# Kernel optimization log

Hardware: AMD Instinct MI355X
Metric: run time of the kernel (lower is better)

The kernel has to match this reference:

```python
import jax, jax.numpy as jnp
import numpy as np

B, S, D, E, H = 65536, 4, 128, 128, 4
HD = E // H
EPS = 1e-5


def setup_inputs() -> dict:
    key = jax.random.key(0)
    ks = jax.random.split(key, 20)
    sc = 0.05
    return {
        'h0': jax.random.normal(ks[0], (B, D), jnp.float32),
        'h1': jax.random.normal(ks[1], (B, D), jnp.float32),
        'h2': jax.random.normal(ks[2], (B, D), jnp.float32),
        'h3': jax.random.normal(ks[3], (B, D), jnp.float32),
        'proj_w': jax.random.normal(ks[4], (S, D, E), jnp.float32) * sc,
        'proj_b': jax.random.normal(ks[5], (S, E), jnp.float32) * sc,
        'ctx_w': jax.random.normal(ks[6], (E,), jnp.float32) * sc,
        'ctx_b': jax.random.normal(ks[7], (), jnp.float32) * sc,
        'in_proj_w': jax.random.normal(ks[8], (E, 3 * E), jnp.float32) * sc,
        'in_proj_b': jax.random.normal(ks[9], (3 * E,), jnp.float32) * sc,
        'out_w': jax.random.normal(ks[10], (E, E), jnp.float32) * sc,
        'out_b': jax.random.normal(ks[11], (E,), jnp.float32) * sc,
        'gate_w': jax.random.normal(ks[12], (2 * E, E), jnp.float32) * sc,
        'gate_b': jax.random.normal(ks[13], (E,), jnp.float32) * sc,
        'pool_w': jax.random.normal(ks[14], (E,), jnp.float32) * sc,
        'pool_b': jax.random.normal(ks[15], (), jnp.float32) * sc,
        'ln_g': jnp.ones((E,), jnp.float32),
        'ln_b': jnp.zeros((E,), jnp.float32),
    }


def reference(h0, h1, h2, h3, proj_w, proj_b, ctx_w, ctx_b, in_proj_w, in_proj_b,
              out_w, out_b, gate_w, gate_b, pool_w, pool_b, ln_g, ln_b):
    hs = jnp.stack([h0, h1, h2, h3], axis=1)                      # [B,S,D]
    x = jnp.einsum('bsd,sde->bse', hs, proj_w) + proj_b           # [B,S,E]
    # context attention over sources
    cw = jax.nn.softmax(x @ ctx_w + ctx_b, axis=1)                # [B,S]
    context = jnp.einsum('bse,bs->be', x, cw)                     # [B,E]
    # single-query MHA: query=context, keys/vals=x
    wq, wk, wv = jnp.split(in_proj_w, 3, axis=1)
    bq, bk, bv = jnp.split(in_proj_b, 3)
    q = (context @ wq + bq).reshape(B, H, HD)
    k = (x @ wk + bk).reshape(B, S, H, HD)
    v = (x @ wv + bv).reshape(B, S, H, HD)
    scores = jnp.einsum('bhd,bshd->bhs', q, k) / jnp.sqrt(jnp.float32(HD))
    attn = jax.nn.softmax(scores, axis=-1)                        # [B,H,S]
    o = jnp.einsum('bhs,bshd->bhd', attn, v).reshape(B, E)
    attn_out = o @ out_w + out_b                                  # [B,E]
    attn_weights = jnp.mean(attn, axis=1)[:, None, :]             # [B,1,S] (avg heads)
    ao = jnp.broadcast_to(attn_out[:, None, :], (B, S, E))
    gate_in = jnp.concatenate([x, ao], axis=-1)                   # [B,S,2E]
    g = jax.nn.sigmoid(gate_in @ gate_w + gate_b)                 # [B,S,E]
    fused = g * ao + (1.0 - g) * x
    mu = fused.mean(axis=-1, keepdims=True)
    var = fused.var(axis=-1, keepdims=True)
    fused = (fused - mu) * jax.lax.rsqrt(var + EPS) * ln_g + ln_b
    pw = jax.nn.softmax(fused @ pool_w + pool_b, axis=1)          # [B,S]
    pooled = jnp.einsum('bse,bs->be', fused, pw)                  # [B,E]
    return pooled, attn_weights, g
```

## Files before the change

kernel.cpp:

```cpp
#include <hip/hip_runtime.h>
#include <hip/hip_bf16.h>

typedef unsigned short u16;
typedef unsigned int   u32;
typedef short  short8 __attribute__((ext_vector_type(8)));
typedef float  f32x4  __attribute__((ext_vector_type(4)));

#define NB    65536
#define XP    132
#define OFF1  ((size_t)NB * 128)
#define OFF2  (OFF1 + (size_t)NB * 4)

__device__ __forceinline__ u16 f2bf(float f) {
  __hip_bfloat16 b = __float2bfloat16(f);
  u16 u; __builtin_memcpy(&u, &b, 2); return u;
}
__device__ __forceinline__ float bf2f(u32 bits16) {
  union { u32 u; float f; } v; v.u = bits16 << 16; return v.f;
}
__device__ __forceinline__ float red16(float v) {
  v += __shfl_xor(v, 1); v += __shfl_xor(v, 2);
  v += __shfl_xor(v, 4); v += __shfl_xor(v, 8);
  return v;
}
__device__ __forceinline__ void lds_fence() {
  asm volatile("s_waitcnt lgkmcnt(0)" ::: "memory");
}

__global__ void pack_w(const float* __restrict__ proj_w,
                       const float* __restrict__ in_proj_w,
                       const float* __restrict__ out_w,
                       const float* __restrict__ gate_w,
                       u16* __restrict__ wp) {
  int t = blockIdx.x * 256 + threadIdx.x;
  if (t >= 10 * 16384) return;
  int w = t >> 14, i = t & 16383;
  int nt = i >> 11, kt = (i >> 9) & 3, ln = (i >> 3) & 63, j = i & 7;
  int k = kt * 32 + ((ln >> 4) << 3) + j;
  int n = (nt << 4) + (ln & 15);
  float v;
  if (w < 4)       v = proj_w[((size_t)w << 14) + (k << 7) + n];
  else if (w < 7)  v = in_proj_w[k * 384 + ((w - 4) << 7) + n];
  else if (w == 7) v = out_w[(k << 7) + n];
  else             v = gate_w[(((w - 8) << 7) + k) * 128 + n];
  wp[t] = f2bf(v);
}

__device__ __forceinline__ short8 bfrag(const u16* __restrict__ wp, int w, int nt, int kt, int lane) {
  return *(const short8*)(wp + ((size_t)w << 14) + (size_t)((((nt << 2) + kt) << 6) + lane) * 8);
}

struct AF { short8 a[4]; };
__device__ __forceinline__ AF loadA(const u16 (*Ab)[XP], int row, int lgrp) {
  AF r;
  #pragma unroll
  for (int kt = 0; kt < 4; ++kt)
    r.a[kt] = *(const short8*)&Ab[row][kt * 32 + (lgrp << 3)];
  return r;
}
__device__ __forceinline__ f32x4 mmK128(const AF& A, const u16* __restrict__ wp, int w,
                                        int ntg, int lane, float bias) {
  f32x4 acc = {bias, bias, bias, bias};
  #pragma unroll
  for (int kt = 0; kt < 4; ++kt)
    acc = __builtin_amdgcn_mfma_f32_16x16x32_bf16(A.a[kt], bfrag(wp, w, ntg, kt, lane), acc, 0, 0, 0);
  return acc;
}

__global__ __launch_bounds__(64, 2) void fused_k(
    const float* __restrict__ h0, const float* __restrict__ h1,
    const float* __restrict__ h2, const float* __restrict__ h3,
    const u16* __restrict__ wp,
    const float* __restrict__ proj_b, const float* __restrict__ ctx_w,
    const float* __restrict__ in_proj_b, const float* __restrict__ out_b,
    const float* __restrict__ gate_b, const float* __restrict__ pool_w,
    const float* __restrict__ ln_g, const float* __restrict__ ln_b,
    float* __restrict__ out) {
  __shared__ __align__(16) u16 xls[4][16][XP];
  __shared__ __align__(16) u16 scr[16][XP];

  const int lane  = threadIdx.x;
  const int lrow  = lane & 15;
  const int lgrp  = lane >> 4;
  const int crow0 = lgrp << 2;
  const size_t r0w = (size_t)blockIdx.x * 16;

  const float* hp[4] = {h0, h1, h2, h3};

  float ctxl[4][4];
  #pragma unroll
  for (int s = 0; s < 4; ++s) {
    const float* __restrict__ hb = hp[s] + ((r0w + lrow) << 7) + (lgrp << 3);
    AF Ah;
    #pragma unroll
    for (int kt = 0; kt < 4; ++kt) {
      float4 va = *(const float4*)(hb + kt * 32);
      float4 vb = *(const float4*)(hb + kt * 32 + 4);
      short8 v;
      v[0] = (short)f2bf(va.x); v[1] = (short)f2bf(va.y);
      v[2] = (short)f2bf(va.z); v[3] = (short)f2bf(va.w);
      v[4] = (short)f2bf(vb.x); v[5] = (short)f2bf(vb.y);
      v[6] = (short)f2bf(vb.z); v[7] = (short)f2bf(vb.w);
      Ah.a[kt] = v;
    }
    float lp[4] = {0.f, 0.f, 0.f, 0.f};
    #pragma unroll
    for (int nt = 0; nt < 8; ++nt) {
      int n = (nt << 4) + lrow;
      f32x4 acc = mmK128(Ah, wp, s, nt, lane, proj_b[(s << 7) + n]);
      float cwn = ctx_w[n];
      #pragma unroll
      for (int j = 0; j < 4; ++j) {
        lp[j] += acc[j] * cwn;
        xls[s][crow0 + j][n] = f2bf(acc[j]);
      }
    }
    #pragma unroll
    for (int j = 0; j < 4; ++j) ctxl[s][j] = red16(lp[j]);
  }

  float cw[4][4];
  #pragma unroll
  for (int j = 0; j < 4; ++j) {
    float l0 = ctxl[0][j], l1 = ctxl[1][j], l2 = ctxl[2][j], l3 = ctxl[3][j];
    float mx = fmaxf(fmaxf(l0, l1), fmaxf(l2, l3));
    float e0 = __expf(l0 - mx), e1 = __expf(l1 - mx), e2 = __expf(l2 - mx), e3 = __expf(l3 - mx);
    float inv = 1.f / (e0 + e1 + e2 + e3);
    cw[0][j] = e0 * inv; cw[1][j] = e1 * inv; cw[2][j] = e2 * inv; cw[3][j] = e3 * inv;
  }
  #pragma unroll
  for (int nt = 0; nt < 8; ++nt) {
    int n = (nt << 4) + lrow;
    #pragma unroll
    for (int j = 0; j < 4; ++j) {
      float v = cw[0][j] * bf2f((u32)xls[0][crow0 + j][n])
              + cw[1][j] * bf2f((u32)xls[1][crow0 + j][n])
              + cw[2][j] * bf2f((u32)xls[2][crow0 + j][n])
              + cw[3][j] * bf2f((u32)xls[3][crow0 + j][n]);
      scr[crow0 + j][n] = f2bf(v);
    }
  }
  lds_fence();
  AF Ac = loadA(scr, lrow, lgrp);

  float qf[8][4];
  #pragma unroll
  for (int nt = 0; nt < 8; ++nt) {
    int n = (nt << 4) + lrow;
    f32x4 acc = mmK128(Ac, wp, 4, nt, lane, in_proj_b[n]);
    #pragma unroll
    for (int j = 0; j < 4; ++j) qf[nt][j] = acc[j];
  }

  lds_fence();
  AF Axs[4];
  #pragma unroll
  for (int s = 0; s < 4; ++s) Axs[s] = loadA(xls[s], lrow, lgrp);
  float sc[4][4][4] = {};
  #pragma unroll
  for (int nt = 0; nt < 8; ++nt) {
    int n = (nt << 4) + lrow;
    const int h = nt >> 1;
    float bk = in_proj_b[128 + n];
    f32x4 ak[4];
    #pragma unroll
    for (int s = 0; s < 4; ++s) ak[s] = (f32x4){bk, bk, bk, bk};
    #pragma unroll
    for (int kt = 0; kt < 4; ++kt) {
      short8 bf = bfrag(wp, 5, nt, kt, lane);
      #pragma unroll
      for (int s = 0; s < 4; ++s)
        ak[s] = __builtin_amdgcn_mfma_f32_16x16x32_bf16(Axs[s].a[kt], bf, ak[s], 0, 0, 0);
    }
    #pragma unroll
    for (int s = 0; s < 4; ++s)
      #pragma unroll
      for (int j = 0; j < 4; ++j)
        sc[s][j][h] += ak[s][j] * qf[nt][j];
  }
  #pragma unroll
  for (int s = 0; s < 4; ++s)
    #pragma unroll
    for (int j = 0; j < 4; ++j)
      #pragma unroll
      for (int h = 0; h < 4; ++h)
        sc[s][j][h] = red16(sc[s][j][h]);

  float aw[4][4][4];
  #pragma unroll
  for (int j = 0; j < 4; ++j)
    #pragma unroll
    for (int h = 0; h < 4; ++h) {
      const float scale = 0.17677669529663687f;
      float l0 = sc[0][j][h] * scale, l1 = sc[1][j][h] * scale;
      float l2 = sc[2][j][h] * scale, l3 = sc[3][j][h] * scale;
      float mx = fmaxf(fmaxf(l0, l1), fmaxf(l2, l3));
      float e0 = __expf(l0 - mx), e1 = __expf(l1 - mx), e2 = __expf(l2 - mx), e3 = __expf(l3 - mx);
      float inv = 1.f / (e0 + e1 + e2 + e3);
      aw[0][j][h] = e0 * inv; aw[1][j][h] = e1 * inv;
      aw[2][j][h] = e2 * inv; aw[3][j][h] = e3 * inv;
    }
  {
    float* awp = (float*)scr;
    if (lrow == 0) {
      #pragma unroll
      for (int s = 0; s < 4; ++s)
        #pragma unroll
        for (int j = 0; j < 4; ++j)
          awp[((crow0 + j) << 2) + s] =
            0.25f * (aw[s][j][0] + aw[s][j][1] + aw[s][j][2] + aw[s][j][3]);
    }
    lds_fence();
    out[OFF1 + (r0w << 2) + lane] = awp[lane];
  }

  {
    float oa[8][4] = {};
    #pragma unroll
    for (int nt = 0; nt < 8; ++nt) {
      int n = (nt << 4) + lrow;
      const int h = nt >> 1;
      float bv = in_proj_b[256 + n];
      f32x4 av[4];
      #pragma unroll
      for (int s = 0; s < 4; ++s) av[s] = (f32x4){bv, bv, bv, bv};
      #pragma unroll
      for (int kt = 0; kt < 4; ++kt) {
        short8 bf = bfrag(wp, 6, nt, kt, lane);
        #pragma unroll
        for (int s = 0; s < 4; ++s)
          av[s] = __builtin_amdgcn_mfma_f32_16x16x32_bf16(Axs[s].a[kt], bf, av[s], 0, 0, 0);
      }
      #pragma unroll
      for (int s = 0; s < 4; ++s)
        #pragma unroll
        for (int j = 0; j < 4; ++j)
          oa[nt][j] += aw[s][j][h] * av[s][j];
    }
    #pragma unroll
    for (int nt = 0; nt < 8; ++nt) {
      int n = (nt << 4) + lrow;
      #pragma unroll
      for (int j = 0; j < 4; ++j) scr[crow0 + j][n] = f2bf(oa[nt][j]);
    }
  }
  lds_fence();
  AF Ao = loadA(scr, lrow, lgrp);

  float aoreg[8][4];
  #pragma unroll
  for (int nt = 0; nt < 8; ++nt) {
    int n = (nt << 4) + lrow;
    f32x4 acc = mmK128(Ao, wp, 7, nt, lane, out_b[n]);
    #pragma unroll
    for (int j = 0; j < 4; ++j) {
      scr[crow0 + j][n] = f2bf(acc[j]);
      aoreg[nt][j] = acc[j];
    }
  }
  lds_fence();
  AF Aa = loadA(scr, lrow, lgrp);

  f32x4 aacc[8];
  #pragma unroll
  for (int nt = 0; nt < 8; ++nt) {
    int n = (nt << 4) + lrow;
    float gb = gate_b[n];
    f32x4 t = {gb, gb, gb, gb};
    #pragma unroll
    for (int kt = 0; kt < 4; ++kt)
      t = __builtin_amdgcn_mfma_f32_16x16x32_bf16(Aa.a[kt], bfrag(wp, 9, nt, kt, lane), t, 0, 0, 0);
    aacc[nt] = t;
  }
  float sm[4][4] = {}, sq[4][4] = {};
  #pragma unroll
  for (int nt = 0; nt < 8; ++nt) {
    int n = (nt << 4) + lrow;
    short8 bf8[4];
    #pragma unroll
    for (int kt = 0; kt < 4; ++kt) bf8[kt] = bfrag(wp, 8, nt, kt, lane);
    #pragma unroll
    for (int s = 0; s < 4; ++s) {
      f32x4 acc = aacc[nt];
      #pragma unroll
      for (int kt = 0; kt < 4; ++kt)
        acc = __builtin_amdgcn_mfma_f32_16x16x32_bf16(Axs[s].a[kt], bf8[kt], acc, 0, 0, 0);
      #pragma unroll
      for (int j = 0; j < 4; ++j) {
        float g = 1.f / (1.f + __expf(-acc[j]));
        out[OFF2 + (((r0w + crow0 + j) << 2) + s) * 128 + n] = g;
        float xv = bf2f((u32)xls[s][crow0 + j][n]);
        float f = g * aoreg[nt][j] + (1.f - g) * xv;
        sm[s][j] += f;
        sq[s][j] += f * f;
        xls[s][crow0 + j][n] = f2bf(f);
      }
    }
  }
  float mean_[4][4], rstd_[4][4];
  #pragma unroll
  for (int s = 0; s < 4; ++s)
    #pragma unroll
    for (int j = 0; j < 4; ++j) {
      float ts = red16(sm[s][j]);
      float tq = red16(sq[s][j]);
      float mean = ts * 0.0078125f;
      float var  = tq * 0.0078125f - mean * mean;
      mean_[s][j] = mean;
      rstd_[s][j] = rsqrtf(var + 1e-5f);
    }

  float lngv[8], lnbv[8], pwvv[8];
  #pragma unroll
  for (int nt = 0; nt < 8; ++nt) {
    int n = (nt << 4) + lrow;
    lngv[nt] = ln_g[n]; lnbv[nt] = ln_b[n]; pwvv[nt] = pool_w[n];
  }
  float pp[4][4] = {};
  #pragma unroll
  for (int nt = 0; nt < 8; ++nt) {
    int n = (nt << 4) + lrow;
    #pragma unroll
    for (int s = 0; s < 4; ++s)
      #pragma unroll
      for (int j = 0; j < 4; ++j) {
        float f  = bf2f((u32)xls[s][crow0 + j][n]);
        float fn = (f - mean_[s][j]) * rstd_[s][j] * lngv[nt] + lnbv[nt];
        pp[s][j] += fn * pwvv[nt];
      }
  }
  float pw[4][4];
  #pragma unroll
  for (int j = 0; j < 4; ++j) {
    float l0 = red16(pp[0][j]), l1 = red16(pp[1][j]);
    float l2 = red16(pp[2][j]), l3 = red16(pp[3][j]);
    float mx = fmaxf(fmaxf(l0, l1), fmaxf(l2, l3));
    float e0 = __expf(l0 - mx), e1 = __expf(l1 - mx), e2 = __expf(l2 - mx), e3 = __expf(l3 - mx);
    float inv = 1.f / (e0 + e1 + e2 + e3);
    pw[0][j] = e0 * inv; pw[1][j] = e1 * inv; pw[2][j] = e2 * inv; pw[3][j] = e3 * inv;
  }
  #pragma unroll
  for (int nt = 0; nt < 8; ++nt) {
    int n = (nt << 4) + lrow;
    #pragma unroll
    for (int j = 0; j < 4; ++j) {
      float acc = 0.f;
      #pragma unroll
      for (int s = 0; s < 4; ++s) {
        float f  = bf2f((u32)xls[s][crow0 + j][n]);
        float fn = (f - mean_[s][j]) * rstd_[s][j] * lngv[nt] + lnbv[nt];
        acc += pw[s][j] * fn;
      }
      out[((r0w + crow0 + j) << 7) + n] = acc;
    }
  }
}

extern "C" void kernel_launch(void* const* d_in, const int* in_sizes, int n_in,
                              void* d_out, int out_size, void* d_ws, size_t ws_size,
                              hipStream_t stream) {
  const float* h0        = (const float*)d_in[0];
  const float* h1        = (const float*)d_in[1];
  const float* h2        = (const float*)d_in[2];
  const float* h3        = (const float*)d_in[3];
  const float* proj_w    = (const float*)d_in[4];
  const float* proj_b    = (const float*)d_in[5];
  const float* ctx_w     = (const float*)d_in[6];
  const float* in_proj_w = (const float*)d_in[8];
  const float* in_proj_b = (const float*)d_in[9];
  const float* out_w     = (const float*)d_in[10];
  const float* out_b     = (const float*)d_in[11];
  const float* gate_w    = (const float*)d_in[12];
  const float* gate_b    = (const float*)d_in[13];
  const float* pool_w    = (const float*)d_in[14];
  const float* ln_g      = (const float*)d_in[16];
  const float* ln_b      = (const float*)d_in[17];
  u16* wp = (u16*)d_ws;

  pack_w<<<640, 256, 0, stream>>>(proj_w, in_proj_w, out_w, gate_w, wp);
  fused_k<<<NB / 16, 64, 0, stream>>>(h0, h1, h2, h3, wp,
                                      proj_b, ctx_w, in_proj_b, out_b, gate_b,
                                      pool_w, ln_g, ln_b, (float*)d_out);
}
```

Measured before the change: 208.2 us.

## Keep projected sources in packed registers instead of LDS, fuse attention per head

Drops the 4x16x132 LDS buffer for the projected sources x. Each lane now keeps its own x and fused values as packed bf16 pairs in registers, and the A-fragments are built once through the single scratch tile. The attention loop is reordered per head so scores, softmax and the value weighting happen together, which drops the large sc/aw/oa arrays. The gate matmul is fused into the fusion loop. This removes LDS traffic and shrinks LDS per block, at the cost of more live registers that may cause spills or lower occupancy.

```diff
diff --git a/kernel.cpp b/kernel.cpp
--- a/kernel.cpp
+++ b/kernel.cpp
@@ -17,6 +17,12 @@
 }
 __device__ __forceinline__ float bf2f(u32 bits16) {
   union { u32 u; float f; } v; v.u = bits16 << 16; return v.f;
+}
+__device__ __forceinline__ u32 pk2(float a, float b) {
+  return (u32)f2bf(a) | ((u32)f2bf(b) << 16);
+}
+__device__ __forceinline__ float unpk(u32 w, int hi) {
+  return bf2f(hi ? (w >> 16) : (w & 0xffffu));
 }
 __device__ __forceinline__ float red16(float v) {
   v += __shfl_xor(v, 1); v += __shfl_xor(v, 2);
@@ -76,7 +82,6 @@
     const float* __restrict__ gate_b, const float* __restrict__ pool_w,
     const float* __restrict__ ln_g, const float* __restrict__ ln_b,
     float* __restrict__ out) {
-  __shared__ __align__(16) u16 xls[4][16][XP];
   __shared__ __align__(16) u16 scr[16][XP];
 
   const int lane  = threadIdx.x;
@@ -88,6 +93,8 @@
   const float* hp[4] = {h0, h1, h2, h3};
 
   float ctxl[4][4];
+  AF Axs[4];
+  u32 xcp[4][8][2];
   #pragma unroll
   for (int s = 0; s < 4; ++s) {
     const float* __restrict__ hb = hp[s] + ((r0w + lrow) << 7) + (lgrp << 3);
@@ -96,12 +103,8 @@
     for (int kt = 0; kt < 4; ++kt) {
       float4 va = *(const float4*)(hb + kt * 32);
       float4 vb = *(const float4*)(hb + kt * 32 + 4);
-      short8 v;
-      v[0] = (short)f2bf(va.x); v[1] = (short)f2bf(va.y);
-      v[2] = (short)f2bf(va.z); v[3] = (short)f2bf(va.w);
-      v[4] = (short)f2bf(vb.x); v[5] = (short)f2bf(vb.y);
-      v[6] = (short)f2bf(vb.z); v[7] = (short)f2bf(vb.w);
-      Ah.a[kt] = v;
+      u32 tmp[4] = {pk2(va.x, va.y), pk2(va.z, va.w), pk2(vb.x, vb.y), pk2(vb.z, vb.w)};
+      __builtin_memcpy(&Ah.a[kt], tmp, 16);
     }
     float lp[4] = {0.f, 0.f, 0.f, 0.f};
     #pragma unroll
@@ -112,114 +115,97 @@
       #pragma unroll
       for (int j = 0; j < 4; ++j) {
         lp[j] += acc[j] * cwn;
-        xls[s][crow0 + j][n] = f2bf(acc[j]);
-      }
+        scr[crow0 + j][n] = f2bf(acc[j]);
+      }
+      xcp[s][nt][0] = pk2(acc[0], acc[1]);
+      xcp[s][nt][1] = pk2(acc[2], acc[3]);
     }
     #pragma unroll
     for (int j = 0; j < 4; ++j) ctxl[s][j] = red16(lp[j]);
-  }
-
-  float cw[4][4];
-  #pragma unroll
-  for (int j = 0; j < 4; ++j) {
-    float l0 = ctxl[0][j], l1 = ctxl[1][j], l2 = ctxl[2][j], l3 = ctxl[3][j];
-    float mx = fmaxf(fmaxf(l0, l1), fmaxf(l2, l3));
-    float e0 = __expf(l0 - mx), e1 = __expf(l1 - mx), e2 = __expf(l2 - mx), e3 = __expf(l3 - mx);
-    float inv = 1.f / (e0 + e1 + e2 + e3);
-    cw[0][j] = e0 * inv; cw[1][j] = e1 * inv; cw[2][j] = e2 * inv; cw[3][j] = e3 * inv;
-  }
-  #pragma unroll
-  for (int nt = 0; nt < 8; ++nt) {
-    int n = (nt << 4) + lrow;
-    #pragma unroll
-    for (int j = 0; j < 4; ++j) {
-      float v = cw[0][j] * bf2f((u32)xls[0][crow0 + j][n])
-              + cw[1][j] * bf2f((u32)xls[1][crow0 + j][n])
-              + cw[2][j] * bf2f((u32)xls[2][crow0 + j][n])
-              + cw[3][j] * bf2f((u32)xls[3][crow0 + j][n]);
-      scr[crow0 + j][n] = f2bf(v);
-    }
-  }
-  lds_fence();
-  AF Ac = loadA(scr, lrow, lgrp);
-
-  float qf[8][4];
-  #pragma unroll
-  for (int nt = 0; nt < 8; ++nt) {
-    int n = (nt << 4) + lrow;
-    f32x4 acc = mmK128(Ac, wp, 4, nt, lane, in_proj_b[n]);
-    #pragma unroll
-    for (int j = 0; j < 4; ++j) qf[nt][j] = acc[j];
-  }
-
-  lds_fence();
-  AF Axs[4];
-  #pragma unroll
-  for (int s = 0; s < 4; ++s) Axs[s] = loadA(xls[s], lrow, lgrp);
-  float sc[4][4][4] = {};
-  #pragma unroll
-  for (int nt = 0; nt < 8; ++nt) {
-    int n = (nt << 4) + lrow;
-    const int h = nt >> 1;
-    float bk = in_proj_b[128 + n];
-    f32x4 ak[4];
-    #pragma unroll
-    for (int s = 0; s < 4; ++s) ak[s] = (f32x4){bk, bk, bk, bk};
-    #pragma unroll
-    for (int kt = 0; kt < 4; ++kt) {
-      short8 bf = bfrag(wp, 5, nt, kt, lane);
-      #pragma unroll
-      for (int s = 0; s < 4; ++s)
-        ak[s] = __builtin_amdgcn_mfma_f32_16x16x32_bf16(Axs[s].a[kt], bf, ak[s], 0, 0, 0);
-    }
-    #pragma unroll
-    for (int s = 0; s < 4; ++s)
-      #pragma unroll
-      for (int j = 0; j < 4; ++j)
-        sc[s][j][h] += ak[s][j] * qf[nt][j];
-  }
-  #pragma unroll
-  for (int s = 0; s < 4; ++s)
-    #pragma unroll
-    for (int j = 0; j < 4; ++j)
-      #pragma unroll
-      for (int h = 0; h < 4; ++h)
-        sc[s][j][h] = red16(sc[s][j][h]);
-
-  float aw[4][4][4];
-  #pragma unroll
-  for (int j = 0; j < 4; ++j)
-    #pragma unroll
-    for (int h = 0; h < 4; ++h) {
-      const float scale = 0.17677669529663687f;
-      float l0 = sc[0][j][h] * scale, l1 = sc[1][j][h] * scale;
-      float l2 = sc[2][j][h] * scale, l3 = sc[3][j][h] * scale;
+    lds_fence();
+    Axs[s] = loadA(scr, lrow, lgrp);
+  }
+
+  {
+    float cw[4][4];
+    #pragma unroll
+    for (int j = 0; j < 4; ++j) {
+      float l0 = ctxl[0][j], l1 = ctxl[1][j], l2 = ctxl[2][j], l3 = ctxl[3][j];
       float mx = fmaxf(fmaxf(l0, l1), fmaxf(l2, l3));
       float e0 = __expf(l0 - mx), e1 = __expf(l1 - mx), e2 = __expf(l2 - mx), e3 = __expf(l3 - mx);
       float inv = 1.f / (e0 + e1 + e2 + e3);
-      aw[0][j][h] = e0 * inv; aw[1][j][h] = e1 * inv;
-      aw[2][j][h] = e2 * inv; aw[3][j][h] = e3 * inv;
-    }
-  {
-    float* awp = (float*)scr;
-    if (lrow == 0) {
+      cw[0][j] = e0 * inv; cw[1][j] = e1 * inv; cw[2][j] = e2 * inv; cw[3][j] = e3 * inv;
+    }
+    #pragma unroll
+    for (int nt = 0; nt < 8; ++nt) {
+      int n = (nt << 4) + lrow;
+      #pragma unroll
+      for (int j = 0; j < 4; ++j) {
+        float v = cw[0][j] * unpk(xcp[0][nt][j >> 1], j & 1)
+                + cw[1][j] * unpk(xcp[1][nt][j >> 1], j & 1)
+                + cw[2][j] * unpk(xcp[2][nt][j >> 1], j & 1)
+                + cw[3][j] * unpk(xcp[3][nt][j >> 1], j & 1);
+        scr[crow0 + j][n] = f2bf(v);
+      }
+    }
+  }
+  lds_fence();
+  AF Ac = loadA(scr, lrow, lgrp);
+
+  float qf[8][4];
+  #pragma unroll
+  for (int nt = 0; nt < 8; ++nt) {
+    int n = (nt << 4) + lrow;
+    f32x4 acc = mmK128(Ac, wp, 4, nt, lane, in_proj_b[n]);
+    #pragma unroll
+    for (int j = 0; j < 4; ++j) qf[nt][j] = acc[j];
+  }
+
+  float awm[4][4] = {};
+  #pragma unroll
+  for (int h = 0; h < 4; ++h) {
+    float sch[4][4] = {};
+    #pragma unroll
+    for (int t = 0; t < 2; ++t) {
+      int nt = (h << 1) + t, n = (nt << 4) + lrow;
+      float bk = in_proj_b[128 + n];
+      f32x4 ak[4];
+      #pragma unroll
+      for (int s = 0; s < 4; ++s) ak[s] = (f32x4){bk, bk, bk, bk};
+      #pragma unroll
+      for (int kt = 0; kt < 4; ++kt) {
+        short8 bf = bfrag(wp, 5, nt, kt, lane);
+        #pragma unroll
+        for (int s = 0; s < 4; ++s)
+          ak[s] = __builtin_amdgcn_mfma_f32_16x16x32_bf16(Axs[s].a[kt], bf, ak[s], 0, 0, 0);
+      }
       #pragma unroll
       for (int s = 0; s < 4; ++s)
         #pragma unroll
         for (int j = 0; j < 4; ++j)
-          awp[((crow0 + j) << 2) + s] =
-            0.25f * (aw[s][j][0] + aw[s][j][1] + aw[s][j][2] + aw[s][j][3]);
-    }
-    lds_fence();
-    out[OFF1 + (r0w << 2) + lane] = awp[lane];
-  }
-
-  {
-    float oa[8][4] = {};
-    #pragma unroll
-    for (int nt = 0; nt < 8; ++nt) {
-      int n = (nt << 4) + lrow;
-      const int h = nt >> 1;
+          sch[s][j] += ak[s][j] * qf[nt][j];
+    }
+    #pragma unroll
+    for (int s = 0; s < 4; ++s)
+      #pragma unroll
+      for (int j = 0; j < 4; ++j)
+        sch[s][j] = red16(sch[s][j]);
+    float awh[4][4];
+    #pragma unroll
+    for (int j = 0; j < 4; ++j) {
+      const float scale = 0.17677669529663687f;
+      float l0 = sch[0][j] * scale, l1 = sch[1][j] * scale;
+      float l2 = sch[2][j] * scale, l3 = sch[3][j] * scale;
+      float mx = fmaxf(fmaxf(l0, l1), fmaxf(l2, l3));
+      float e0 = __expf(l0 - mx), e1 = __expf(l1 - mx), e2 = __expf(l2 - mx), e3 = __expf(l3 - mx);
+      float inv = 1.f / (e0 + e1 + e2 + e3);
+      awh[0][j] = e0 * inv; awh[1][j] = e1 * inv; awh[2][j] = e2 * inv; awh[3][j] = e3 * inv;
+      awm[0][j] += awh[0][j]; awm[1][j] += awh[1][j];
+      awm[2][j] += awh[2][j]; awm[3][j] += awh[3][j];
+    }
+    #pragma unroll
+    for (int t = 0; t < 2; ++t) {
+      int nt = (h << 1) + t, n = (nt << 4) + lrow;
       float bv = in_proj_b[256 + n];
       f32x4 av[4];
       #pragma unroll
@@ -232,20 +218,28 @@
           av[s] = __builtin_amdgcn_mfma_f32_16x16x32_bf16(Axs[s].a[kt], bf, av[s], 0, 0, 0);
       }
       #pragma unroll
+      for (int j = 0; j < 4; ++j) {
+        float oj = awh[0][j] * av[0][j] + awh[1][j] * av[1][j]
+                 + awh[2][j] * av[2][j] + awh[3][j] * av[3][j];
+        scr[crow0 + j][n] = f2bf(oj);
+      }
+    }
+  }
+  lds_fence();
+  AF Ao = loadA(scr, lrow, lgrp);
+
+  {
+    float* awp = (float*)scr;
+    if (lrow == 0) {
+      #pragma unroll
       for (int s = 0; s < 4; ++s)
         #pragma unroll
         for (int j = 0; j < 4; ++j)
-          oa[nt][j] += aw[s][j][h] * av[s][j];
-    }
-    #pragma unroll
-    for (int nt = 0; nt < 8; ++nt) {
-      int n = (nt << 4) + lrow;
-      #pragma unroll
-      for (int j = 0; j < 4; ++j) scr[crow0 + j][n] = f2bf(oa[nt][j]);
-    }
-  }
-  lds_fence();
-  AF Ao = loadA(scr, lrow, lgrp);
+          awp[((crow0 + j) << 2) + s] = 0.25f * awm[s][j];
+    }
+    lds_fence();
+    out[OFF1 + (r0w << 2) + lane] = awp[lane];
+  }
 
   float aoreg[8][4];
   #pragma unroll
@@ -261,40 +255,36 @@
   lds_fence();
   AF Aa = loadA(scr, lrow, lgrp);
 
-  f32x4 aacc[8];
+  float sm[4][4] = {}, sq[4][4] = {};
   #pragma unroll
   for (int nt = 0; nt < 8; ++nt) {
     int n = (nt << 4) + lrow;
     float gb = gate_b[n];
-    f32x4 t = {gb, gb, gb, gb};
+    f32x4 tt = {gb, gb, gb, gb};
     #pragma unroll
     for (int kt = 0; kt < 4; ++kt)
-      t = __builtin_amdgcn_mfma_f32_16x16x32_bf16(Aa.a[kt], bfrag(wp, 9, nt, kt, lane), t, 0, 0, 0);
-    aacc[nt] = t;
-  }
-  float sm[4][4] = {}, sq[4][4] = {};
-  #pragma unroll
-  for (int nt = 0; nt < 8; ++nt) {
-    int n = (nt << 4) + lrow;
+      tt = __builtin_amdgcn_mfma_f32_16x16x32_bf16(Aa.a[kt], bfrag(wp, 9, nt, kt, lane), tt, 0, 0, 0);
     short8 bf8[4];
     #pragma unroll
     for (int kt = 0; kt < 4; ++kt) bf8[kt] = bfrag(wp, 8, nt, kt, lane);
     #pragma unroll
     for (int s = 0; s < 4; ++s) {
-      f32x4 acc = aacc[nt];
+      f32x4 acc = tt;
       #pragma unroll
       for (int kt = 0; kt < 4; ++kt)
         acc = __builtin_amdgcn_mfma_f32_16x16x32_bf16(Axs[s].a[kt], bf8[kt], acc, 0, 0, 0);
+      float f[4];
       #pragma unroll
       for (int j = 0; j < 4; ++j) {
         float g = 1.f / (1.f + __expf(-acc[j]));
         out[OFF2 + (((r0w + crow0 + j) << 2) + s) * 128 + n] = g;
-        float xv = bf2f((u32)xls[s][crow0 + j][n]);
-        float f = g * aoreg[nt][j] + (1.f - g) * xv;
-        sm[s][j] += f;
-        sq[s][j] += f * f;
-        xls[s][crow0 + j][n] = f2bf(f);
-      }
+        float xv = unpk(xcp[s][nt][j >> 1], j & 1);
+        f[j] = g * aoreg[nt][j] + (1.f - g) * xv;
+        sm[s][j] += f[j];
+        sq[s][j] += f[j] * f[j];
+      }
+      xcp[s][nt][0] = pk2(f[0], f[1]);
+      xcp[s][nt][1] = pk2(f[2], f[3]);
     }
   }
   float mean_[4][4], rstd_[4][4];
@@ -319,12 +309,11 @@
   float pp[4][4] = {};
   #pragma unroll
   for (int nt = 0; nt < 8; ++nt) {
-    int n = (nt << 4) + lrow;
     #pragma unroll
     for (int s = 0; s < 4; ++s)
       #pragma unroll
       for (int j = 0; j < 4; ++j) {
-        float f  = bf2f((u32)xls[s][crow0 + j][n]);
+        float f  = unpk(xcp[s][nt][j >> 1], j & 1);
         float fn = (f - mean_[s][j]) * rstd_[s][j] * lngv[nt] + lnbv[nt];
         pp[s][j] += fn * pwvv[nt];
       }
@@ -347,7 +336,7 @@
       float acc = 0.f;
       #pragma unroll
       for (int s = 0; s < 4; ++s) {
-        float f  = bf2f((u32)xls[s][crow0 + j][n]);
+        float f  = unpk(xcp[s][nt][j >> 1], j & 1);
         float fn = (f - mean_[s][j]) * rstd_[s][j] * lngv[nt] + lnbv[nt];
         acc += pw[s][j] * fn;
       }
```

Measured after the change: 598.3 us. 187% more time.

## Keep source-0 projection in registers to shrink LDS footprint

Applied to the files above, without the earlier changes.

Source 0's projected activations now live in packed bf16 registers (xcp0) and its MFMA A fragment is loaded early from the scratch buffer, so the LDS activation array drops from four sources to three. The launch-bounds minimum-occupancy hint is removed, giving the compiler more register headroom. Smaller LDS per block is meant to allow more resident wavefronts and cut LDS traffic. In exchange, register pressure rises: Axs[0] and xcp0 are held across the whole kernel, which may cause spills or lower occupancy.

```diff
diff --git a/kernel.cpp b/kernel.cpp
--- a/kernel.cpp
+++ b/kernel.cpp
@@ -17,6 +17,12 @@
 }
 __device__ __forceinline__ float bf2f(u32 bits16) {
   union { u32 u; float f; } v; v.u = bits16 << 16; return v.f;
+}
+__device__ __forceinline__ u32 pk2(float a, float b) {
+  return (u32)f2bf(a) | ((u32)f2bf(b) << 16);
+}
+__device__ __forceinline__ float unpk(u32 w, int hi) {
+  return bf2f(hi ? (w >> 16) : (w & 0xffffu));
 }
 __device__ __forceinline__ float red16(float v) {
   v += __shfl_xor(v, 1); v += __shfl_xor(v, 2);
@@ -67,7 +73,7 @@
   return acc;
 }
 
-__global__ __launch_bounds__(64, 2) void fused_k(
+__global__ __launch_bounds__(64) void fused_k(
     const float* __restrict__ h0, const float* __restrict__ h1,
     const float* __restrict__ h2, const float* __restrict__ h3,
     const u16* __restrict__ wp,
@@ -76,7 +82,7 @@
     const float* __restrict__ gate_b, const float* __restrict__ pool_w,
     const float* __restrict__ ln_g, const float* __restrict__ ln_b,
     float* __restrict__ out) {
-  __shared__ __align__(16) u16 xls[4][16][XP];
+  __shared__ __align__(16) u16 xls[3][16][XP];
   __shared__ __align__(16) u16 scr[16][XP];
 
   const int lane  = threadIdx.x;
@@ -88,6 +94,8 @@
   const float* hp[4] = {h0, h1, h2, h3};
 
   float ctxl[4][4];
+  AF Axs[4];
+  u32 xcp0[8][2];
   #pragma unroll
   for (int s = 0; s < 4; ++s) {
     const float* __restrict__ hb = hp[s] + ((r0w + lrow) << 7) + (lgrp << 3);
@@ -96,12 +104,8 @@
     for (int kt = 0; kt < 4; ++kt) {
       float4 va = *(const float4*)(hb + kt * 32);
       float4 vb = *(const float4*)(hb + kt * 32 + 4);
-      short8 v;
-      v[0] = (short)f2bf(va.x); v[1] = (short)f2bf(va.y);
-      v[2] = (short)f2bf(va.z); v[3] = (short)f2bf(va.w);
-      v[4] = (short)f2bf(vb.x); v[5] = (short)f2bf(vb.y);
-      v[6] = (short)f2bf(vb.z); v[7] = (short)f2bf(vb.w);
-      Ah.a[kt] = v;
+      u32 tmp[4] = {pk2(va.x, va.y), pk2(va.z, va.w), pk2(vb.x, vb.y), pk2(vb.z, vb.w)};
+      __builtin_memcpy(&Ah.a[kt], tmp, 16);
     }
     float lp[4] = {0.f, 0.f, 0.f, 0.f};
     #pragma unroll
@@ -112,11 +116,20 @@
       #pragma unroll
       for (int j = 0; j < 4; ++j) {
         lp[j] += acc[j] * cwn;
-        xls[s][crow0 + j][n] = f2bf(acc[j]);
+        if (s == 0) scr[crow0 + j][n] = f2bf(acc[j]);
+        else        xls[s - 1][crow0 + j][n] = f2bf(acc[j]);
+      }
+      if (s == 0) {
+        xcp0[nt][0] = pk2(acc[0], acc[1]);
+        xcp0[nt][1] = pk2(acc[2], acc[3]);
       }
     }
     #pragma unroll
     for (int j = 0; j < 4; ++j) ctxl[s][j] = red16(lp[j]);
+    if (s == 0) {
+      lds_fence();
+      Axs[0] = loadA(scr, lrow, lgrp);
+    }
   }
 
   float cw[4][4];
@@ -133,10 +146,10 @@
     int n = (nt << 4) + lrow;
     #pragma unroll
     for (int j = 0; j < 4; ++j) {
-      float v = cw[0][j] * bf2f((u32)xls[0][crow0 + j][n])
-              + cw[1][j] * bf2f((u32)xls[1][crow0 + j][n])
-              + cw[2][j] * bf2f((u32)xls[2][crow0 + j][n])
-              + cw[3][j] * bf2f((u32)xls[3][crow0 + j][n]);
+      float v = cw[0][j] * unpk(xcp0[nt][j >> 1], j & 1)
+              + cw[1][j] * bf2f((u32)xls[0][crow0 + j][n])
+              + cw[2][j] * bf2f((u32)xls[1][crow0 + j][n])
+              + cw[3][j] * bf2f((u32)xls[2][crow0 + j][n]);
       scr[crow0 + j][n] = f2bf(v);
     }
   }
@@ -153,9 +166,8 @@
   }
 
   lds_fence();
-  AF Axs[4];
-  #pragma unroll
-  for (int s = 0; s < 4; ++s) Axs[s] = loadA(xls[s], lrow, lgrp);
+  #pragma unroll
+  for (int s = 1; s < 4; ++s) Axs[s] = loadA(xls[s - 1], lrow, lgrp);
   float sc[4][4][4] = {};
   #pragma unroll
   for (int nt = 0; nt < 8; ++nt) {
@@ -285,15 +297,21 @@
       #pragma unroll
       for (int kt = 0; kt < 4; ++kt)
         acc = __builtin_amdgcn_mfma_f32_16x16x32_bf16(Axs[s].a[kt], bf8[kt], acc, 0, 0, 0);
+      float f[4];
       #pragma unroll
       for (int j = 0; j < 4; ++j) {
         float g = 1.f / (1.f + __expf(-acc[j]));
         out[OFF2 + (((r0w + crow0 + j) << 2) + s) * 128 + n] = g;
-        float xv = bf2f((u32)xls[s][crow0 + j][n]);
-        float f = g * aoreg[nt][j] + (1.f - g) * xv;
-        sm[s][j] += f;
-        sq[s][j] += f * f;
-        xls[s][crow0 + j][n] = f2bf(f);
+        float xv = (s == 0) ? unpk(xcp0[nt][j >> 1], j & 1)
+                            : bf2f((u32)xls[s - 1][crow0 + j][n]);
+        f[j] = g * aoreg[nt][j] + (1.f - g) * xv;
+        sm[s][j] += f[j];
+        sq[s][j] += f[j] * f[j];
+        if (s > 0) xls[s - 1][crow0 + j][n] = f2bf(f[j]);
+      }
+      if (s == 0) {
+        xcp0[nt][0] = pk2(f[0], f[1]);
+        xcp0[nt][1] = pk2(f[2], f[3]);
       }
     }
   }
@@ -324,7 +342,8 @@
     for (int s = 0; s < 4; ++s)
       #pragma unroll
       for (int j = 0; j < 4; ++j) {
-        float f  = bf2f((u32)xls[s][crow0 + j][n]);
+        float f  = (s == 0) ? unpk(xcp0[nt][j >> 1], j & 1)
+                            : bf2f((u32)xls[s - 1][crow0 + j][n]);
         float fn = (f - mean_[s][j]) * rstd_[s][j] * lngv[nt] + lnbv[nt];
         pp[s][j] += fn * pwvv[nt];
       }
@@ -347,7 +366,8 @@
       float acc = 0.f;
       #pragma unroll
       for (int s = 0; s < 4; ++s) {
-        float f  = bf2f((u32)xls[s][crow0 + j][n]);
+        float f  = (s == 0) ? unpk(xcp0[nt][j >> 1], j & 1)
+                            : bf2f((u32)xls[s - 1][crow0 + j][n]);
         float fn = (f - mean_[s][j]) * rstd_[s][j] * lngv[nt] + lnbv[nt];
         acc += pw[s][j] * fn;
       }
```

Measured after the change: 202.7 us. 1.03x faster.
